# Kernel tuning notes

Measured on AMD Instinct MI355X. Metric: run time of the kernel, lower is better.

## Reference

```python
import jax, jax.numpy as jnp
import numpy as np
import math

N, CIN, COUT, K, H, W = 16, 512, 512, 1024, 64, 64


def setup_inputs() -> dict:
    key = jax.random.key(0)
    k0, k1, k2, k3, k4 = jax.random.split(key, 5)
    latent = jax.random.normal(k0, (N, CIN, H, W), dtype=jnp.float32)
    # kaiming_uniform_ on (K, COUT): bound = sqrt(6 / fan_in), fan_in = COUT
    cb_bound = math.sqrt(6.0 / COUT)
    codebook = jax.random.uniform(k1, (K, COUT), minval=-cb_bound, maxval=cb_bound, dtype=jnp.float32)
    # nn.Linear default init: uniform(-1/sqrt(fan_in), 1/sqrt(fan_in)), weight stored (out, in)
    wq = jax.random.uniform(k2, (COUT, CIN), minval=-1 / math.sqrt(CIN), maxval=1 / math.sqrt(CIN), dtype=jnp.float32)
    wk = jax.random.uniform(k3, (COUT, COUT), minval=-1 / math.sqrt(COUT), maxval=1 / math.sqrt(COUT), dtype=jnp.float32)
    wv = jax.random.uniform(k4, (COUT, COUT), minval=-1 / math.sqrt(COUT), maxval=1 / math.sqrt(COUT), dtype=jnp.float32)
    return {"latent": latent, "codebook": codebook, "wq": wq, "wk": wk, "wv": wv, "temperature": 1}


def _forward(latent, codebook, wq, wk, wv, temperature):
    n, cin, h, w = latent.shape
    kk, cout = codebook.shape
    scale = math.sqrt(cin)

    q = jnp.einsum("nchw,oc->nhwo", latent, wq)          # [n,h,w,cout]
    kmat = codebook @ wk.T                                   # [k,cout]
    v = codebook @ wv.T                                      # [k,cout]
    logit = jnp.einsum("nhwc,kc->nhwk", q, kmat) / scale  # [n,h,w,k]

    # ---- no-grad mask / histogram computation (dropout branch) ----
    lg = jax.lax.stop_gradient(logit)
    rk = jax.random.key(1234)
    r1, r2, r3 = jax.random.split(rk, 3)
    prob = jax.nn.softmax(lg, axis=-1)
    prob = jnp.where(prob < 1.0 / kk, 0.0, prob)
    mask = jax.random.bernoulli(r1, prob)                    # [n,h,w,k] bool
    trueCode = jnp.argmax(prob, axis=-1)                     # [n,h,w] int
    flat = trueCode.reshape(n, -1)
    binCount = jnp.zeros((n, kk), dtype=jnp.float32).at[jnp.arange(n)[:, None], flat].add(1.0)
    frequency = binCount[jnp.arange(n)[:, None, None], trueCode]  # [n,h,w]
    dropout = jax.random.bernoulli(r2, frequency / float(h * w))   # [n,h,w] bool
    scatterMask = jax.nn.one_hot(trueCode, kk, dtype=jnp.bool_) & dropout[..., None]
    mask = mask | scatterMask

    maskedLogit = jnp.where(mask, -1e9, logit)

    # ---- hard gumbel-softmax (straight-through) ----
    g = jax.random.gumbel(r3, maskedLogit.shape, dtype=maskedLogit.dtype)
    y_soft = jax.nn.softmax((maskedLogit + g) / temperature, axis=-1)
    y_hard = jax.nn.one_hot(jnp.argmax(y_soft, axis=-1), kk, dtype=y_soft.dtype)
    sample = y_hard - jax.lax.stop_gradient(y_soft) + y_soft

    result = jnp.einsum("nhwk,kc->nhwc", sample, v)
    quantized = jnp.transpose(result, (0, 3, 1, 2))          # [n,cout,h,w]
    code = jnp.argmax(sample, axis=-1)
    return quantized, code, logit, trueCode, frequency, binCount


def reference(latent, codebook, wq, wk, wv, temperature):
    return _forward(latent, codebook, wq, wk, wv, temperature)
```

## Files before the change

kernel.cpp:

```cpp
#include <hip/hip_runtime.h>
#include <stdint.h>
#include <stddef.h>

#define NB   16
#define CIN  512
#define COUT 512
#define KK   1024

#define MARGIN    2e-5f
#define INV_SCALE 0.04419417382415922f

typedef short short4v __attribute__((ext_vector_type(4)));
typedef short short8v __attribute__((ext_vector_type(8)));
typedef float f32x4  __attribute__((ext_vector_type(4)));

union Frag { short4v h[2]; short8v v8; };

__host__ __device__ inline void tf2x32(uint32_t k0, uint32_t k1,
                                       uint32_t x0, uint32_t x1,
                                       uint32_t& o0, uint32_t& o1) {
  uint32_t ks2 = k0 ^ k1 ^ 0x1BD11BDAu;
  x0 += k0; x1 += k1;
#define TF_RND(r) { x0 += x1; x1 = (x1 << r) | (x1 >> (32 - r)); x1 ^= x0; }
  TF_RND(13) TF_RND(15) TF_RND(26) TF_RND(6)
  x0 += k1;  x1 += ks2 + 1u;
  TF_RND(17) TF_RND(29) TF_RND(16) TF_RND(24)
  x0 += ks2; x1 += k0 + 2u;
  TF_RND(13) TF_RND(15) TF_RND(26) TF_RND(6)
  x0 += k0;  x1 += k1 + 3u;
  TF_RND(17) TF_RND(29) TF_RND(16) TF_RND(24)
  x0 += k1;  x1 += ks2 + 4u;
  TF_RND(13) TF_RND(15) TF_RND(26) TF_RND(6)
  x0 += ks2; x1 += k0 + 5u;
#undef TF_RND
  o0 = x0; o1 = x1;
}

__device__ inline float bits_to_u(uint32_t b) {
  return __uint_as_float((b >> 9) | 0x3f800000u) - 1.0f;
}

__device__ __host__ inline uint16_t f2bf(float f) {
  union { float f; uint32_t u; } c; c.f = f;
  uint32_t r = (c.u + 0x7fffu + ((c.u >> 16) & 1u)) >> 16;
  return (uint16_t)r;
}
__device__ inline float bf2f(uint16_t h) {
  union { uint32_t u; float f; } c; c.u = ((uint32_t)h) << 16;
  return c.f;
}

__device__ inline int permpos(int c) {
  const int base32 = c & ~31, within = c & 31;
  const int g = (within >> 2) & 3;
  const int e = (within & 16) ? (4 + (within & 3)) : (within & 3);
  return base32 + g * 8 + e;
}

__global__ __launch_bounds__(256) void k_prep(const float* __restrict__ cb,
                                              const float* __restrict__ wk,
                                              const float* __restrict__ wv,
                                              double* __restrict__ kmatT64,
                                              float* __restrict__ v) {
  __shared__ __align__(16) float rows[4][CIN];
  const int k0 = blockIdx.x * 4;
  const int t = threadIdx.x;
#pragma unroll
  for (int kk = 0; kk < 4; ++kk)
    for (int c = t; c < CIN; c += 256) rows[kk][c] = cb[(size_t)(k0 + kk) * CIN + c];
  __syncthreads();
#pragma unroll
  for (int oo = 0; oo < 2; ++oo) {
    const int o = t + oo * 256;
    const float* kr = wk + (size_t)o * CIN;
    const float* vr = wv + (size_t)o * CIN;
    double ak[4] = {0, 0, 0, 0}, av[4] = {0, 0, 0, 0};
    for (int c = 0; c < CIN; c += 4) {
      const float4 k4 = *(const float4*)(kr + c);
      const float4 v4 = *(const float4*)(vr + c);
#pragma unroll
      for (int kk = 0; kk < 4; ++kk) {
        const float4 c4 = *(const float4*)&rows[kk][c];
        ak[kk] += (double)c4.x * (double)k4.x + (double)c4.y * (double)k4.y
                + (double)c4.z * (double)k4.z + (double)c4.w * (double)k4.w;
        av[kk] += (double)c4.x * (double)v4.x + (double)c4.y * (double)v4.y
                + (double)c4.z * (double)v4.z + (double)c4.w * (double)v4.w;
      }
    }
#pragma unroll
    for (int kk = 0; kk < 4; ++kk) {
      kmatT64[(size_t)o * KK + k0 + kk] = ak[kk];
      v[(size_t)(k0 + kk) * COUT + o]  = (float)av[kk];
    }
  }
}

__global__ __launch_bounds__(256) void k_wfold(const float* __restrict__ wq,
                                               const double* __restrict__ kmatT64,
                                               double* __restrict__ WT64,
                                               uint16_t* __restrict__ Wph,
                                               uint16_t* __restrict__ Wpl) {
  __shared__ __align__(16) float  As[16][64];
  __shared__ __align__(16) double Bs[16][128];
  const int t  = threadIdx.x;
  const int cb = (blockIdx.x >> 3) * 64;
  const int kb = (blockIdx.x & 7) * 128;
  const int tc = t >> 4, tk = t & 15;

  double acc[4][8];
#pragma unroll
  for (int i = 0; i < 4; ++i)
#pragma unroll
    for (int j = 0; j < 8; ++j) acc[i][j] = 0.0;

  for (int o0 = 0; o0 < COUT; o0 += 16) {
    {
      const int o2 = t >> 4, c4 = (t & 15) * 4;
      float4 f = *(const float4*)&wq[(size_t)(o0 + o2) * CIN + cb + c4];
      As[o2][c4+0] = f.x; As[o2][c4+1] = f.y; As[o2][c4+2] = f.z; As[o2][c4+3] = f.w;
    }
    {
      const int o2 = t >> 4, k8 = (t & 15) * 8;
      const double* src = &kmatT64[(size_t)(o0 + o2) * KK + kb + k8];
#pragma unroll
      for (int j = 0; j < 8; ++j) Bs[o2][k8 + j] = src[j];
    }
    __syncthreads();
#pragma unroll 4
    for (int o2 = 0; o2 < 16; ++o2) {
      double a[4], b[8];
#pragma unroll
      for (int i = 0; i < 4; ++i) a[i] = (double)As[o2][tc*4 + i];
#pragma unroll
      for (int j = 0; j < 8; ++j) b[j] = Bs[o2][tk*8 + j];
#pragma unroll
      for (int i = 0; i < 4; ++i)
#pragma unroll
        for (int j = 0; j < 8; ++j) acc[i][j] += a[i] * b[j];
    }
    __syncthreads();
  }
#pragma unroll
  for (int i = 0; i < 4; ++i) {
    const int c = cb + tc*4 + i;
    const int pp = permpos(c);
#pragma unroll
    for (int j = 0; j < 8; ++j) {
      const int k = kb + tk*8 + j;
      const double a = acc[i][j];
      WT64[(size_t)k * CIN + c] = a;
      const float wf = (float)a;
      const uint16_t hb = f2bf(wf);
      const float lof = wf - bf2f(hb);
      Wph[(size_t)k * CIN + pp] = hb;
      Wpl[(size_t)k * CIN + pp] = f2bf(lof);
    }
  }
}

__global__ __launch_bounds__(256) void k_aprep(const float* __restrict__ latent,
                                               uint16_t* __restrict__ Apk) {
  __shared__ float T[128][68];
  const int rb = blockIdx.x, n = rb >> 6, h = rb & 63, t = threadIdx.x;
  for (int c0 = 0; c0 < 512; c0 += 128) {
    const int c2 = t >> 1, wh = (t & 1) * 32;
    const float* src = latent + (size_t)n * 2097152 + (size_t)(c0 + c2) * 4096 + h * 64 + wh;
#pragma unroll
    for (int i = 0; i < 8; ++i)
      *(float4*)&T[c2][wh + i*4] = *(const float4*)(src + i*4);
    __syncthreads();
    const int w = t & 63, cp = t >> 6;
    const int cs = (c0 >> 5) + cp;
    const int p = rb * 64 + w;
    uint16_t* dst = Apk + ((size_t)cs * 65536 + p) * 64;
#pragma unroll
    for (int q = 0; q < 8; ++q) {
      short8v vv;
#pragma unroll
      for (int j = 0; j < 4; ++j) {
        const float f = T[cp*32 + (q & 3) * 4 + (q >> 2) * 16 + j][w];
        const uint16_t hb = f2bf(f);
        vv[j]     = (short)hb;
        vv[4 + j] = (short)f2bf(f - bf2f(hb));
      }
      *(short8v*)(dst + q * 8) = vv;
    }
    __syncthreads();
  }
}

#define STAGE_B(buf_, st_) do {                                            \
  const int kc_ = (st_) >> 4, cs_ = (st_) & 15;                            \
  _Pragma("unroll")                                                        \
  for (int i_ = 0; i_ < 8; ++i_) {                                         \
    const int half_ = i_ >> 2;                                             \
    const int Dl_ = (i_ & 3) * 4096 + wave * 1024 + lane * 16;             \
    const int kcol_ = Dl_ >> 6;                                            \
    const int bs_ = ((Dl_ >> 4) & 3) ^ ((kcol_ >> 1) & 3);                 \
    const uint16_t* gsrc_ = (half_ ? Wpl : Wph) +                          \
        ((size_t)(kc_ * 256 + kcol_) * 512 + cs_ * 32 + bs_ * 8);          \
    uint16_t* ldst_ = &Bst[buf_][half_ * 8192 + (Dl_ >> 1)];               \
    __builtin_amdgcn_global_load_lds(                                      \
        (const __attribute__((address_space(1))) uint32_t*)gsrc_,          \
        (__attribute__((address_space(3))) uint32_t*)ldst_, 16, 0, 0);     \
  } } while (0)

#define STAGE_A(buf_, st_) do {                                            \
  const int cs_ = (st_) & 15;                                              \
  _Pragma("unroll")                                                        \
  for (int i_ = 0; i_ < 2; ++i_) {                                         \
    const int D_ = i_ * 4096 + t * 16;                                     \
    const int row_ = D_ >> 7;                                              \
    const int q_ = ((D_ >> 4) & 7) ^ (row_ & 7);                           \
    const uint16_t* gsrc_ = Apk +                                          \
        ((size_t)cs_ * 65536 + pbase + row_) * 64 + q_ * 8;                \
    uint16_t* ldst_ = &Ast[buf_][D_ >> 1];                                 \
    __builtin_amdgcn_global_load_lds(                                      \
        (const __attribute__((address_space(1))) uint32_t*)gsrc_,          \
        (__attribute__((address_space(3))) uint32_t*)ldst_, 16, 0, 0);     \
  } } while (0)

__global__ __launch_bounds__(256, 2) void k_logit(
    const uint16_t* __restrict__ Apk,
    const uint16_t* __restrict__ Wph, const uint16_t* __restrict__ Wpl,
    const float* __restrict__ latent, const double* __restrict__ WT64,
    float* __restrict__ out_logit, int* __restrict__ trueCode, int* __restrict__ binCnt) {
  __shared__ __align__(16) char smem[81920];
  uint16_t (*Bst)[16384] = (uint16_t(*)[16384])smem;
  uint16_t (*Ast)[4096]  = (uint16_t(*)[4096])(smem + 65536);
  float* rowBv   = (float*)(smem + 65536);
  int*   rowBk   = (int*)  (smem + 65536 + 256);
  int*   candCnt = (int*)  (smem + 65536 + 512);
  int  (*candK)[8] = (int(*)[8])(smem + 65536 + 768);

  const int t = threadIdx.x;
  const int wave = t >> 6, lane = t & 63;
  const int wr = wave >> 1, wc = wave & 1;
  const int rb = blockIdx.x, n = rb >> 6, h = rb & 63;
  const int pbase = rb * 64;
  const int lg = lane >> 4, l15 = lane & 15;

  float bestv[2][4]; int bestk[2][4];
#pragma unroll
  for (int rt = 0; rt < 2; ++rt)
#pragma unroll
    for (int reg = 0; reg < 4; ++reg) { bestv[rt][reg] = -1.0e30f; bestk[rt][reg] = 0; }

  f32x4 acc[2][8];

  STAGE_A(0, 0);
  STAGE_B(0, 0);
  __syncthreads();

  for (int st = 0; st < 64; ++st) {
    const int cur = st & 1, kc = st >> 4, cs = st & 15;
    if (cs == 0) {
#pragma unroll
      for (int rt = 0; rt < 2; ++rt)
#pragma unroll
        for (int ct = 0; ct < 8; ++ct) acc[rt][ct] = (f32x4){0.f, 0.f, 0.f, 0.f};
    }
    if (st < 63) { STAGE_A(cur ^ 1, st + 1); STAGE_B(cur ^ 1, st + 1); }

    Frag ah[2], al[2];
#pragma unroll
    for (int rt = 0; rt < 2; ++rt) {
      const int row = wr * 32 + rt * 16 + l15;
      const uint16_t* ab = &Ast[cur][row * 64];
      const int s0 = (lg ^ (row & 7)) * 8;
      Frag f0, f1;
      f0.v8 = *(const short8v*)(ab + s0);
      f1.v8 = *(const short8v*)(ab + (s0 ^ 32));
      ah[rt].h[0] = f0.h[0]; ah[rt].h[1] = f1.h[0];
      al[rt].h[0] = f0.h[1]; al[rt].h[1] = f1.h[1];
    }

#pragma unroll
    for (int ct = 0; ct < 8; ++ct) {
      const int kcol = wc * 128 + ct * 16 + l15;
      const int sw = lg ^ ((kcol >> 1) & 3);
      Frag bh, bl;
      bh.v8 = *(const short8v*)&Bst[cur][kcol * 32 + sw * 8];
      bl.v8 = *(const short8v*)&Bst[cur][8192 + kcol * 32 + sw * 8];
#pragma unroll
      for (int rt = 0; rt < 2; ++rt) {
        acc[rt][ct] = __builtin_amdgcn_mfma_f32_16x16x32_bf16(ah[rt].v8, bh.v8, acc[rt][ct], 0, 0, 0);
        acc[rt][ct] = __builtin_amdgcn_mfma_f32_16x16x32_bf16(ah[rt].v8, bl.v8, acc[rt][ct], 0, 0, 0);
        acc[rt][ct] = __builtin_amdgcn_mfma_f32_16x16x32_bf16(al[rt].v8, bh.v8, acc[rt][ct], 0, 0, 0);
      }
    }
    if (cs == 15) {
#pragma unroll
      for (int rt = 0; rt < 2; ++rt) {
#pragma unroll
        for (int reg = 0; reg < 4; ++reg) {
          const int prow = pbase + wr * 32 + rt * 16 + 4 * lg + reg;
          float* dst = out_logit + (size_t)prow * KK + kc * 256 + wc * 128 + l15;
#pragma unroll
          for (int ct = 0; ct < 8; ++ct) {
            const float v = acc[rt][ct][reg] * INV_SCALE;
            dst[ct * 16] = v;
            if (v > bestv[rt][reg]) { bestv[rt][reg] = v; bestk[rt][reg] = kc * 256 + wc * 128 + ct * 16 + l15; }
          }
        }
      }
    }
    __syncthreads();
  }

#pragma unroll
  for (int rt = 0; rt < 2; ++rt)
#pragma unroll
    for (int reg = 0; reg < 4; ++reg) {
      float v = bestv[rt][reg]; int k = bestk[rt][reg];
#pragma unroll
      for (int off = 1; off < 16; off <<= 1) {
        const float ov = __shfl_xor(v, off);
        const int   ok = __shfl_xor(k, off);
        if (ov > v || (ov == v && ok < k)) { v = ov; k = ok; }
      }
      bestv[rt][reg] = v; bestk[rt][reg] = k;
    }
  if (l15 == 0 && wc == 0) {
#pragma unroll
    for (int rt = 0; rt < 2; ++rt)
#pragma unroll
      for (int reg = 0; reg < 4; ++reg) {
        const int r = wr * 32 + rt * 16 + 4 * lg + reg;
        rowBv[r] = bestv[rt][reg]; rowBk[r] = bestk[rt][reg];
      }
  }
  if (t < 64) candCnt[t] = 0;
  __syncthreads();
  if (l15 == 0 && wc == 1) {
#pragma unroll
    for (int rt = 0; rt < 2; ++rt)
#pragma unroll
      for (int reg = 0; reg < 4; ++reg) {
        const int r = wr * 32 + rt * 16 + 4 * lg + reg;
        const float v = bestv[rt][reg]; const int k = bestk[rt][reg];
        if (v > rowBv[r] || (v == rowBv[r] && k < rowBk[r])) { rowBv[r] = v; rowBk[r] = k; }
      }
  }
  __syncthreads();

  {
    const int r = t >> 2, qd = t & 3;
    const size_t base = (size_t)(pbase + r) * KK + qd * 256;
    const float thr = rowBv[r] - MARGIN;
    for (int x = 0; x < 64; ++x) {
      const float4 f = *(const float4*)&out_logit[base + x * 4];
      const int kb = qd * 256 + x * 4;
      if (f.x >= thr) { int id = atomicAdd(&candCnt[r], 1); if (id < 8) candK[r][id] = kb + 0; }
      if (f.y >= thr) { int id = atomicAdd(&candCnt[r], 1); if (id < 8) candK[r][id] = kb + 1; }
      if (f.z >= thr) { int id = atomicAdd(&candCnt[r], 1); if (id < 8) candK[r][id] = kb + 2; }
      if (f.w >= thr) { int id = atomicAdd(&candCnt[r], 1); if (id < 8) candK[r][id] = kb + 3; }
    }
  }
  __syncthreads();

  const float* Ab = latent + (size_t)n * CIN * 4096 + h * 64;
  const int wv = t >> 6, lane_ = t & 63;
  for (int rr = 0; rr < 16; ++rr) {
    const int r = wv * 16 + rr;
    const int p = pbase + r;
    int cnt = candCnt[r]; if (cnt > 8) cnt = 8;
    if (cnt <= 1) {
      if (lane_ == 0) {
        const int tc0 = rowBk[r];
        trueCode[p] = tc0;
        atomicAdd(&binCnt[n * KK + tc0], 1);
      }
    } else {
      int ks[8];
#pragma unroll
      for (int m = 0; m < 8; ++m) ks[m] = candK[r][m < cnt ? m : 0];
      double part[8] = {0, 0, 0, 0, 0, 0, 0, 0};
#pragma unroll
      for (int jj = 0; jj < 8; ++jj) {
        const int c = jj * 64 + lane_;
        const double lv = (double)Ab[(size_t)c * 4096 + r];
#pragma unroll
        for (int m = 0; m < 8; ++m)
          if (m < cnt) part[m] += lv * WT64[(size_t)ks[m] * CIN + c];
      }
#pragma unroll
      for (int m = 0; m < 8; ++m)
        for (int off = 32; off; off >>= 1) part[m] += __shfl_xor(part[m], off);
      if (lane_ == 0) {
        double bv = -1.0e300; int bkk = KK;
#pragma unroll
        for (int m = 0; m < 8; ++m)
          if (m < cnt && (part[m] > bv || (part[m] == bv && ks[m] < bkk))) { bv = part[m]; bkk = ks[m]; }
        trueCode[p] = bkk;
        atomicAdd(&binCnt[n * KK + bkk], 1);
      }
    }
  }
}

__global__ __launch_bounds__(256) void k_final(const float* __restrict__ logit,
                                               const int* __restrict__ trueCode,
                                               const int* __restrict__ binCnt,
                                               float* __restrict__ out_code,
                                               float* __restrict__ out_tc,
                                               float* __restrict__ out_freq,
                                               int* __restrict__ code_int,
                                               uint32_t r1a, uint32_t r1b,
                                               uint32_t r2a, uint32_t r2b,
                                               uint32_t r3a, uint32_t r3b) {
  const int lane = threadIdx.x & 63;
  const int p = blockIdx.x * 4 + (threadIdx.x >> 6);
  const float* Lr = logit + (size_t)p * KK + lane * 16;

  float l[16];
#pragma unroll
  for (int i = 0; i < 4; ++i) {
    const float4 f = *(const float4*)(Lr + i * 4);
    l[i*4+0] = f.x; l[i*4+1] = f.y; l[i*4+2] = f.z; l[i*4+3] = f.w;
  }

  float m = l[0];
#pragma unroll
  for (int i = 1; i < 16; ++i) m = fmaxf(m, l[i]);
  for (int off = 32; off; off >>= 1) m = fmaxf(m, __shfl_xor(m, off));

  float e[16], s = 0.f;
#pragma unroll
  for (int i = 0; i < 16; ++i) { e[i] = __expf(l[i] - m); s += e[i]; }
  for (int off = 32; off; off >>= 1) s += __shfl_xor(s, off);

  const int tc = trueCode[p];
  const float fq = (float)binCnt[(p >> 12) * KK + tc];
  uint32_t d0, d1; tf2x32(r2a, r2b, 0u, (uint32_t)p, d0, d1);
  const bool drop = bits_to_u(d0 ^ d1) < fq * (1.0f / 4096.0f);

  const float thr = s * 0.0009765625f;
  float bv = -3.0e38f; int bk = 0;
#pragma unroll
  for (int j = 0; j < 16; ++j) {
    const int k = lane * 16 + j;
    const uint32_t idx = (uint32_t)(p * KK + k);
    uint32_t m0, m1, g0, g1;
    tf2x32(r1a, r1b, 0u, idx, m0, m1);
    tf2x32(r3a, r3b, 0u, idx, g0, g1);
    const bool mk = ((e[j] >= thr) && (bits_to_u(m0 ^ m1) * s < e[j])) || (k == tc && drop);
    const float u3  = fmaxf(bits_to_u(g0 ^ g1), 1.17549435082228751e-38f);
    const float gum = -__logf(-logf(u3));
    const float z = mk ? (gum - 1.0e9f) : (l[j] + gum);
    if (z > bv) { bv = z; bk = k; }
  }
  for (int off = 32; off; off >>= 1) {
    const float ov = __shfl_xor(bv, off);
    const int   ok = __shfl_xor(bk, off);
    if (ov > bv || (ov == bv && ok < bk)) { bv = ov; bk = ok; }
  }
  if (lane == 0) {
    out_code[p] = (float)bk; code_int[p] = bk;
    out_tc[p] = (float)tc;   out_freq[p] = fq;
  }
}

__global__ __launch_bounds__(256) void k_quant(const float* __restrict__ v,
                                               const int* __restrict__ code_int,
                                               float* __restrict__ outq) {
  const int rb = blockIdx.x;
  const int n = rb >> 6, h = rb & 63;
  const int t = threadIdx.x;
  __shared__ int codes[64];
  if (t < 64) codes[t] = code_int[rb * 64 + t];
  __syncthreads();
  const int w = t & 63, og = t >> 6;
  const float* vr = v + (size_t)codes[w] * COUT;
  float* ob = outq + (size_t)n * COUT * 4096 + (size_t)h * 64 + w;
  for (int o = og * 128; o < og * 128 + 128; ++o)
    ob[(size_t)o * 4096] = vr[o];
}

__global__ __launch_bounds__(256) void k_bincopy(const int* __restrict__ binCnt,
                                                 float* __restrict__ outb) {
  const int i = blockIdx.x * 256 + threadIdx.x;
  if (i < NB * KK) outb[i] = (float)binCnt[i];
}

extern "C" void kernel_launch(void* const* d_in, const int* in_sizes, int n_in,
                              void* d_out, int out_size, void* d_ws, size_t ws_size,
                              hipStream_t stream) {
  const float* latent   = (const float*)d_in[0];
  const float* codebook = (const float*)d_in[1];
  const float* wq       = (const float*)d_in[2];
  const float* wk       = (const float*)d_in[3];
  const float* wv       = (const float*)d_in[4];

  float* out = (float*)d_out;
  float* out_quant = out;
  float* out_code  = out + 33554432;
  float* out_logit = out + 33619968;
  float* out_tc    = out + 100728832;
  float* out_freq  = out + 100794368;
  float* out_bin   = out + 100859904;

  double*   WT64 = (double*)  out_quant;
  uint16_t* Wph  = (uint16_t*)(out_quant + 1048576);
  uint16_t* Wpl  = (uint16_t*)(out_quant + 1310720);

  char* ws = (char*)d_ws;
  uint16_t* Apk     = (uint16_t*)(ws);
  double*   kmatT64 = (double*)(ws);
  float*    v       = (float*)(ws + 134217728);
  int*      trueCode= (int*)  (ws + 136314880);
  int*      code_int= (int*)  (ws + 136577024);
  int*      binCnt  = (int*)  (ws + 136839168);

  uint32_t r1a, r1b, r2a, r2b, r3a, r3b;
  tf2x32(0u, 1234u, 0u, 0u, r1a, r1b);
  tf2x32(0u, 1234u, 0u, 1u, r2a, r2b);
  tf2x32(0u, 1234u, 0u, 2u, r3a, r3b);

  hipMemsetAsync(binCnt, 0, NB * KK * sizeof(int), stream);
  k_prep  <<<256,   256, 0, stream>>>(codebook, wk, wv, kmatT64, v);
  k_wfold <<<64,    256, 0, stream>>>(wq, kmatT64, WT64, Wph, Wpl);
  k_aprep <<<1024,  256, 0, stream>>>(latent, Apk);
  k_logit <<<1024,  256, 0, stream>>>(Apk, Wph, Wpl, latent, WT64,
                                      out_logit, trueCode, binCnt);
  k_final <<<16384, 256, 0, stream>>>(out_logit, trueCode, binCnt,
                                      out_code, out_tc, out_freq, code_int,
                                      r1a, r1b, r2a, r2b, r3a, r3b);
  k_quant <<<1024,  256, 0, stream>>>(v, code_int, out_quant);
  k_bincopy<<<64,   256, 0, stream>>>(binCnt, out_bin);
}
```

Before: 988.9 us.

## Fuse codebook prep with latent packing, track top-2 logits, coalesce quant writes

Merges the codebook projection kernel and the latent bf16 packing kernel into one launch, with kmatT64 moved into the output buffer so it no longer aliases Apk in the workspace. The logit kernel now tracks the top-2 logits per row and only rescans the logit row when the gap is under the margin, which skips the full candidate scan for most rows. The quantize kernel is restructured so each block writes contiguous float4 runs along the spatial axis. The cost is more registers for the top-2 bookkeeping and a gather pattern on v in the quant kernel.

```diff
diff --git a/kernel.cpp b/kernel.cpp
--- a/kernel.cpp
+++ b/kernel.cpp
@@ -57,40 +57,73 @@
   return base32 + g * 8 + e;
 }
 
-__global__ __launch_bounds__(256) void k_prep(const float* __restrict__ cb,
-                                              const float* __restrict__ wk,
-                                              const float* __restrict__ wv,
-                                              double* __restrict__ kmatT64,
-                                              float* __restrict__ v) {
-  __shared__ __align__(16) float rows[4][CIN];
-  const int k0 = blockIdx.x * 4;
+__global__ __launch_bounds__(256) void k_combo(const float* __restrict__ cb,
+                                               const float* __restrict__ wk,
+                                               const float* __restrict__ wv,
+                                               const float* __restrict__ latent,
+                                               double* __restrict__ kmatT64,
+                                               float* __restrict__ v,
+                                               uint16_t* __restrict__ Apk) {
+  __shared__ __align__(16) char sm[34816];
   const int t = threadIdx.x;
-#pragma unroll
-  for (int kk = 0; kk < 4; ++kk)
-    for (int c = t; c < CIN; c += 256) rows[kk][c] = cb[(size_t)(k0 + kk) * CIN + c];
-  __syncthreads();
-#pragma unroll
-  for (int oo = 0; oo < 2; ++oo) {
-    const int o = t + oo * 256;
-    const float* kr = wk + (size_t)o * CIN;
-    const float* vr = wv + (size_t)o * CIN;
-    double ak[4] = {0, 0, 0, 0}, av[4] = {0, 0, 0, 0};
-    for (int c = 0; c < CIN; c += 4) {
-      const float4 k4 = *(const float4*)(kr + c);
-      const float4 v4 = *(const float4*)(vr + c);
-#pragma unroll
-      for (int kk = 0; kk < 4; ++kk) {
-        const float4 c4 = *(const float4*)&rows[kk][c];
-        ak[kk] += (double)c4.x * (double)k4.x + (double)c4.y * (double)k4.y
-                + (double)c4.z * (double)k4.z + (double)c4.w * (double)k4.w;
-        av[kk] += (double)c4.x * (double)v4.x + (double)c4.y * (double)v4.y
-                + (double)c4.z * (double)v4.z + (double)c4.w * (double)v4.w;
-      }
-    }
-#pragma unroll
-    for (int kk = 0; kk < 4; ++kk) {
-      kmatT64[(size_t)o * KK + k0 + kk] = ak[kk];
-      v[(size_t)(k0 + kk) * COUT + o]  = (float)av[kk];
+  if (blockIdx.x < 128) {
+    float (*rows)[CIN] = (float(*)[CIN])sm;
+    const int k0 = blockIdx.x * 8;
+#pragma unroll
+    for (int kk = 0; kk < 8; ++kk)
+      for (int c = t; c < CIN; c += 256) rows[kk][c] = cb[(size_t)(k0 + kk) * CIN + c];
+    __syncthreads();
+#pragma unroll
+    for (int oo = 0; oo < 2; ++oo) {
+      const int o = t + oo * 256;
+      const float* kr = wk + (size_t)o * CIN;
+      const float* vr = wv + (size_t)o * CIN;
+      double ak[8] = {0,0,0,0,0,0,0,0}, av[8] = {0,0,0,0,0,0,0,0};
+      for (int c = 0; c < CIN; c += 4) {
+        const float4 k4 = *(const float4*)(kr + c);
+        const float4 v4 = *(const float4*)(vr + c);
+#pragma unroll
+        for (int kk = 0; kk < 8; ++kk) {
+          const float4 c4 = *(const float4*)&rows[kk][c];
+          ak[kk] += (double)c4.x * (double)k4.x + (double)c4.y * (double)k4.y
+                  + (double)c4.z * (double)k4.z + (double)c4.w * (double)k4.w;
+          av[kk] += (double)c4.x * (double)v4.x + (double)c4.y * (double)v4.y
+                  + (double)c4.z * (double)v4.z + (double)c4.w * (double)v4.w;
+        }
+      }
+#pragma unroll
+      for (int kk = 0; kk < 8; ++kk) {
+        kmatT64[(size_t)o * KK + k0 + kk] = ak[kk];
+        v[(size_t)(k0 + kk) * COUT + o]  = (float)av[kk];
+      }
+    }
+  } else {
+    float (*T)[68] = (float(*)[68])sm;
+    const int rb = blockIdx.x - 128, n = rb >> 6, h = rb & 63;
+    for (int c0 = 0; c0 < 512; c0 += 128) {
+      const int c2 = t >> 1, wh = (t & 1) * 32;
+      const float* src = latent + (size_t)n * 2097152 + (size_t)(c0 + c2) * 4096 + h * 64 + wh;
+#pragma unroll
+      for (int i = 0; i < 8; ++i)
+        *(float4*)&T[c2][wh + i*4] = *(const float4*)(src + i*4);
+      __syncthreads();
+      const int w = t & 63, cp = t >> 6;
+      const int cs = (c0 >> 5) + cp;
+      const int p = rb * 64 + w;
+      uint16_t* dst = Apk + ((size_t)cs * 65536 + p) * 64;
+#pragma unroll
+      for (int q = 0; q < 8; ++q) {
+        short8v vv;
+#pragma unroll
+        for (int j = 0; j < 4; ++j) {
+          const float f = T[cp*32 + (q & 3) * 4 + (q >> 2) * 16 + j][w];
+          const uint16_t hb = f2bf(f);
+          vv[j]     = (short)hb;
+          vv[4 + j] = (short)f2bf(f - bf2f(hb));
+        }
+        *(short8v*)(dst + q * 8) = vv;
+      }
+      __syncthreads();
     }
   }
 }
@@ -158,48 +191,17 @@
   }
 }
 
-__global__ __launch_bounds__(256) void k_aprep(const float* __restrict__ latent,
-                                               uint16_t* __restrict__ Apk) {
-  __shared__ float T[128][68];
-  const int rb = blockIdx.x, n = rb >> 6, h = rb & 63, t = threadIdx.x;
-  for (int c0 = 0; c0 < 512; c0 += 128) {
-    const int c2 = t >> 1, wh = (t & 1) * 32;
-    const float* src = latent + (size_t)n * 2097152 + (size_t)(c0 + c2) * 4096 + h * 64 + wh;
-#pragma unroll
-    for (int i = 0; i < 8; ++i)
-      *(float4*)&T[c2][wh + i*4] = *(const float4*)(src + i*4);
-    __syncthreads();
-    const int w = t & 63, cp = t >> 6;
-    const int cs = (c0 >> 5) + cp;
-    const int p = rb * 64 + w;
-    uint16_t* dst = Apk + ((size_t)cs * 65536 + p) * 64;
-#pragma unroll
-    for (int q = 0; q < 8; ++q) {
-      short8v vv;
-#pragma unroll
-      for (int j = 0; j < 4; ++j) {
-        const float f = T[cp*32 + (q & 3) * 4 + (q >> 2) * 16 + j][w];
-        const uint16_t hb = f2bf(f);
-        vv[j]     = (short)hb;
-        vv[4 + j] = (short)f2bf(f - bf2f(hb));
-      }
-      *(short8v*)(dst + q * 8) = vv;
-    }
-    __syncthreads();
-  }
-}
-
 #define STAGE_B(buf_, st_) do {                                            \
   const int kc_ = (st_) >> 4, cs_ = (st_) & 15;                            \
   _Pragma("unroll")                                                        \
   for (int i_ = 0; i_ < 8; ++i_) {                                         \
     const int half_ = i_ >> 2;                                             \
-    const int Dl_ = (i_ & 3) * 4096 + wave * 1024 + lane * 16;             \
-    const int kcol_ = Dl_ >> 6;                                            \
-    const int bs_ = ((Dl_ >> 4) & 3) ^ ((kcol_ >> 1) & 3);                 \
+    const int D_ = (i_ & 3) * 4096 + wave * 1024 + lane * 16;              \
+    const int kcol_ = D_ >> 6;                                             \
+    const int bs_ = ((D_ >> 4) & 3) ^ ((kcol_ >> 1) & 3);                  \
     const uint16_t* gsrc_ = (half_ ? Wpl : Wph) +                          \
         ((size_t)(kc_ * 256 + kcol_) * 512 + cs_ * 32 + bs_ * 8);          \
-    uint16_t* ldst_ = &Bst[buf_][half_ * 8192 + (Dl_ >> 1)];               \
+    uint16_t* ldst_ = &Bst[buf_][half_ * 8192 + (D_ >> 1)];                \
     __builtin_amdgcn_global_load_lds(                                      \
         (const __attribute__((address_space(1))) uint32_t*)gsrc_,          \
         (__attribute__((address_space(3))) uint32_t*)ldst_, 16, 0, 0);     \
@@ -228,23 +230,28 @@
   __shared__ __align__(16) char smem[81920];
   uint16_t (*Bst)[16384] = (uint16_t(*)[16384])smem;
   uint16_t (*Ast)[4096]  = (uint16_t(*)[4096])(smem + 65536);
-  float* rowBv   = (float*)(smem + 65536);
-  int*   rowBk   = (int*)  (smem + 65536 + 256);
-  int*   candCnt = (int*)  (smem + 65536 + 512);
-  int  (*candK)[8] = (int(*)[8])(smem + 65536 + 768);
+  float* rv1     = (float*)(smem + 65536);
+  int*   rk1     = (int*)  (smem + 65536 + 256);
+  float* rv2     = (float*)(smem + 65536 + 512);
+  int*   rk2     = (int*)  (smem + 65536 + 768);
+  int*   candCnt = (int*)  (smem + 65536 + 1024);
+  int  (*candK)[8] = (int(*)[8])(smem + 65536 + 1280);
 
   const int t = threadIdx.x;
   const int wave = t >> 6, lane = t & 63;
   const int wr = wave >> 1, wc = wave & 1;
-  const int rb = blockIdx.x, n = rb >> 6, h = rb & 63;
+  const int rb = blockIdx.x, n = rb >> 6;
   const int pbase = rb * 64;
   const int lg = lane >> 4, l15 = lane & 15;
 
-  float bestv[2][4]; int bestk[2][4];
+  float v1_[2][4], v2_[2][4]; int k1_[2][4], k2_[2][4];
 #pragma unroll
   for (int rt = 0; rt < 2; ++rt)
 #pragma unroll
-    for (int reg = 0; reg < 4; ++reg) { bestv[rt][reg] = -1.0e30f; bestk[rt][reg] = 0; }
+    for (int reg = 0; reg < 4; ++reg) {
+      v1_[rt][reg] = -3.0e38f; k1_[rt][reg] = 0x7fffffff;
+      v2_[rt][reg] = -3.0e38f; k2_[rt][reg] = 0x7fffffff;
+    }
 
   f32x4 acc[2][8];
 
@@ -296,12 +303,18 @@
         for (int reg = 0; reg < 4; ++reg) {
           const int prow = pbase + wr * 32 + rt * 16 + 4 * lg + reg;
           float* dst = out_logit + (size_t)prow * KK + kc * 256 + wc * 128 + l15;
+          float v1 = v1_[rt][reg], v2 = v2_[rt][reg];
+          int   k1 = k1_[rt][reg], k2 = k2_[rt][reg];
 #pragma unroll
           for (int ct = 0; ct < 8; ++ct) {
-            const float v = acc[rt][ct][reg] * INV_SCALE;
-            dst[ct * 16] = v;
-            if (v > bestv[rt][reg]) { bestv[rt][reg] = v; bestk[rt][reg] = kc * 256 + wc * 128 + ct * 16 + l15; }
+            const float vv = acc[rt][ct][reg] * INV_SCALE;
+            dst[ct * 16] = vv;
+            const int kk = kc * 256 + wc * 128 + ct * 16 + l15;
+            if (vv > v1 || (vv == v1 && kk < k1)) { v2 = v1; k2 = k1; v1 = vv; k1 = kk; }
+            else if (vv > v2 || (vv == v2 && kk < k2)) { v2 = vv; k2 = kk; }
           }
+          v1_[rt][reg] = v1; v2_[rt][reg] = v2;
+          k1_[rt][reg] = k1; k2_[rt][reg] = k2;
         }
       }
     }
@@ -312,66 +325,99 @@
   for (int rt = 0; rt < 2; ++rt)
 #pragma unroll
     for (int reg = 0; reg < 4; ++reg) {
-      float v = bestv[rt][reg]; int k = bestk[rt][reg];
+      float v1 = v1_[rt][reg], v2 = v2_[rt][reg];
+      int   k1 = k1_[rt][reg], k2 = k2_[rt][reg];
 #pragma unroll
       for (int off = 1; off < 16; off <<= 1) {
-        const float ov = __shfl_xor(v, off);
-        const int   ok = __shfl_xor(k, off);
-        if (ov > v || (ov == v && ok < k)) { v = ov; k = ok; }
-      }
-      bestv[rt][reg] = v; bestk[rt][reg] = k;
-    }
-  if (l15 == 0 && wc == 0) {
+        const float o1 = __shfl_xor(v1, off); const int ok1 = __shfl_xor(k1, off);
+        const float o2 = __shfl_xor(v2, off); const int ok2 = __shfl_xor(k2, off);
+        const bool aw = (v1 > o1) || (v1 == o1 && k1 < ok1);
+        float n1, n2; int nk1, nk2;
+        if (aw) {
+          n1 = v1; nk1 = k1;
+          if ((o1 > v2) || (o1 == v2 && ok1 < k2)) { n2 = o1; nk2 = ok1; }
+          else { n2 = v2; nk2 = k2; }
+        } else {
+          n1 = o1; nk1 = ok1;
+          if ((v1 > o2) || (v1 == o2 && k1 < ok2)) { n2 = v1; nk2 = k1; }
+          else { n2 = o2; nk2 = ok2; }
+        }
+        v1 = n1; k1 = nk1; v2 = n2; k2 = nk2;
+      }
+      v1_[rt][reg] = v1; v2_[rt][reg] = v2;
+      k1_[rt][reg] = k1; k2_[rt][reg] = k2;
+    }
+  if (wc == 0 && l15 == 0) {
 #pragma unroll
     for (int rt = 0; rt < 2; ++rt)
 #pragma unroll
       for (int reg = 0; reg < 4; ++reg) {
         const int r = wr * 32 + rt * 16 + 4 * lg + reg;
-        rowBv[r] = bestv[rt][reg]; rowBk[r] = bestk[rt][reg];
-      }
-  }
-  if (t < 64) candCnt[t] = 0;
+        rv1[r] = v1_[rt][reg]; rk1[r] = k1_[rt][reg];
+        rv2[r] = v2_[rt][reg]; rk2[r] = k2_[rt][reg];
+      }
+  }
   __syncthreads();
-  if (l15 == 0 && wc == 1) {
+  if (wc == 1 && l15 == 0) {
 #pragma unroll
     for (int rt = 0; rt < 2; ++rt)
 #pragma unroll
       for (int reg = 0; reg < 4; ++reg) {
         const int r = wr * 32 + rt * 16 + 4 * lg + reg;
-        const float v = bestv[rt][reg]; const int k = bestk[rt][reg];
-        if (v > rowBv[r] || (v == rowBv[r] && k < rowBk[r])) { rowBv[r] = v; rowBk[r] = k; }
+        const float a1 = rv1[r], a2 = rv2[r];
+        const int   ak1 = rk1[r], ak2 = rk2[r];
+        const float b1 = v1_[rt][reg], b2 = v2_[rt][reg];
+        const int   bk1 = k1_[rt][reg], bk2 = k2_[rt][reg];
+        const bool aw = (a1 > b1) || (a1 == b1 && ak1 < bk1);
+        float n1, n2; int nk1, nk2;
+        if (aw) {
+          n1 = a1; nk1 = ak1;
+          if ((b1 > a2) || (b1 == a2 && bk1 < ak2)) { n2 = b1; nk2 = bk1; }
+          else { n2 = a2; nk2 = ak2; }
+        } else {
+          n1 = b1; nk1 = bk1;
+          if ((a1 > b2) || (a1 == b2 && ak1 < bk2)) { n2 = a1; nk2 = ak1; }
+          else { n2 = b2; nk2 = bk2; }
+        }
+        rv1[r] = n1; rk1[r] = nk1; rv2[r] = n2; rk2[r] = nk2;
       }
   }
   __syncthreads();
 
-  {
-    const int r = t >> 2, qd = t & 3;
-    const size_t base = (size_t)(pbase + r) * KK + qd * 256;
-    const float thr = rowBv[r] - MARGIN;
-    for (int x = 0; x < 64; ++x) {
-      const float4 f = *(const float4*)&out_logit[base + x * 4];
-      const int kb = qd * 256 + x * 4;
-      if (f.x >= thr) { int id = atomicAdd(&candCnt[r], 1); if (id < 8) candK[r][id] = kb + 0; }
-      if (f.y >= thr) { int id = atomicAdd(&candCnt[r], 1); if (id < 8) candK[r][id] = kb + 1; }
-      if (f.z >= thr) { int id = atomicAdd(&candCnt[r], 1); if (id < 8) candK[r][id] = kb + 2; }
-      if (f.w >= thr) { int id = atomicAdd(&candCnt[r], 1); if (id < 8) candK[r][id] = kb + 3; }
-    }
-  }
-  __syncthreads();
-
-  const float* Ab = latent + (size_t)n * CIN * 4096 + h * 64;
   const int wv = t >> 6, lane_ = t & 63;
   for (int rr = 0; rr < 16; ++rr) {
     const int r = wv * 16 + rr;
     const int p = pbase + r;
-    int cnt = candCnt[r]; if (cnt > 8) cnt = 8;
-    if (cnt <= 1) {
+    const float mv1 = rv1[r], mv2 = rv2[r];
+    if (mv1 - mv2 > MARGIN) {
       if (lane_ == 0) {
-        const int tc0 = rowBk[r];
+        const int tc0 = rk1[r];
         trueCode[p] = tc0;
         atomicAdd(&binCnt[n * KK + tc0], 1);
       }
     } else {
+      if (lane_ == 0) candCnt[r] = 0;
+      __builtin_amdgcn_sched_barrier(0);
+      asm volatile("s_waitcnt lgkmcnt(0)" ::: "memory");
+      __builtin_amdgcn_sched_barrier(0);
+      {
+        const float thr = mv1 - MARGIN;
+        const float* src = out_logit + (size_t)p * KK + lane_ * 16;
+#pragma unroll
+        for (int i = 0; i < 4; ++i) {
+          const float4 f = *(const float4*)(src + i * 4);
+          const int kb = lane_ * 16 + i * 4;
+          if (f.x >= thr) { int id = atomicAdd(&candCnt[r], 1); if (id < 8) candK[r][id] = kb + 0; }
+          if (f.y >= thr) { int id = atomicAdd(&candCnt[r], 1); if (id < 8) candK[r][id] = kb + 1; }
+          if (f.z >= thr) { int id = atomicAdd(&candCnt[r], 1); if (id < 8) candK[r][id] = kb + 2; }
+          if (f.w >= thr) { int id = atomicAdd(&candCnt[r], 1); if (id < 8) candK[r][id] = kb + 3; }
+        }
+      }
+      __builtin_amdgcn_sched_barrier(0);
+      asm volatile("s_waitcnt lgkmcnt(0)" ::: "memory");
+      __builtin_amdgcn_sched_barrier(0);
+      int cnt = candCnt[r]; if (cnt > 8) cnt = 8;
+      const float* Ap = latent + (size_t)(p >> 12) * 2097152 + (p & 4095);
       int ks[8];
 #pragma unroll
       for (int m = 0; m < 8; ++m) ks[m] = candK[r][m < cnt ? m : 0];
@@ -379,7 +425,7 @@
 #pragma unroll
       for (int jj = 0; jj < 8; ++jj) {
         const int c = jj * 64 + lane_;
-        const double lv = (double)Ab[(size_t)c * 4096 + r];
+        const double lv = (double)Ap[(size_t)c * 4096];
 #pragma unroll
         for (int m = 0; m < 8; ++m)
           if (m < cnt) part[m] += lv * WT64[(size_t)ks[m] * CIN + c];
@@ -464,17 +510,29 @@
 __global__ __launch_bounds__(256) void k_quant(const float* __restrict__ v,
                                                const int* __restrict__ code_int,
                                                float* __restrict__ outq) {
-  const int rb = blockIdx.x;
-  const int n = rb >> 6, h = rb & 63;
+  __shared__ int codes[4096];
+  const int n  = blockIdx.x >> 6;
+  const int og = blockIdx.x & 63;
   const int t = threadIdx.x;
-  __shared__ int codes[64];
-  if (t < 64) codes[t] = code_int[rb * 64 + t];
+  const int4* cp = (const int4*)(code_int + (size_t)n * 4096);
+#pragma unroll
+  for (int i = 0; i < 4; ++i) ((int4*)codes)[t + i * 256] = cp[t + i * 256];
   __syncthreads();
-  const int w = t & 63, og = t >> 6;
-  const float* vr = v + (size_t)codes[w] * COUT;
-  float* ob = outq + (size_t)n * COUT * 4096 + (size_t)h * 64 + w;
-  for (int o = og * 128; o < og * 128 + 128; ++o)
-    ob[(size_t)o * 4096] = vr[o];
+  float* ob = outq + ((size_t)n * 512 + og * 8) * 4096;
+  for (int c = 0; c < 4; ++c) {
+    const int pos4 = (c * 256 + t) * 4;
+    const int c0 = codes[pos4], c1 = codes[pos4 + 1], c2 = codes[pos4 + 2], c3 = codes[pos4 + 3];
+    const float* v0 = v + (size_t)c0 * COUT;
+    const float* v1 = v + (size_t)c1 * COUT;
+    const float* v2 = v + (size_t)c2 * COUT;
+    const float* v3 = v + (size_t)c3 * COUT;
+#pragma unroll
+    for (int oo = 0; oo < 8; ++oo) {
+      const int o = og * 8 + oo;
+      float4 val = make_float4(v0[o], v1[o], v2[o], v3[o]);
+      *(float4*)(ob + (size_t)oo * 4096 + pos4) = val;
+    }
+  }
 }
 
 __global__ __launch_bounds__(256) void k_bincopy(const int* __restrict__ binCnt,
@@ -500,13 +558,13 @@
   float* out_freq  = out + 100794368;
   float* out_bin   = out + 100859904;
 
-  double*   WT64 = (double*)  out_quant;
-  uint16_t* Wph  = (uint16_t*)(out_quant + 1048576);
-  uint16_t* Wpl  = (uint16_t*)(out_quant + 1310720);
+  double*   WT64    = (double*)  out_quant;
+  uint16_t* Wph     = (uint16_t*)(out_quant + 1048576);
+  uint16_t* Wpl     = (uint16_t*)(out_quant + 1310720);
+  double*   kmatT64 = (double*)  (out_quant + 1572864);
 
   char* ws = (char*)d_ws;
   uint16_t* Apk     = (uint16_t*)(ws);
-  double*   kmatT64 = (double*)(ws);
   float*    v       = (float*)(ws + 134217728);
   int*      trueCode= (int*)  (ws + 136314880);
   int*      code_int= (int*)  (ws + 136577024);
@@ -518,9 +576,8 @@
   tf2x32(0u, 1234u, 0u, 2u, r3a, r3b);
 
   hipMemsetAsync(binCnt, 0, NB * KK * sizeof(int), stream);
-  k_prep  <<<256,   256, 0, stream>>>(codebook, wk, wv, kmatT64, v);
+  k_combo <<<1152,  256, 0, stream>>>(codebook, wk, wv, latent, kmatT64, v, Apk);
   k_wfold <<<64,    256, 0, stream>>>(wq, kmatT64, WT64, Wph, Wpl);
-  k_aprep <<<1024,  256, 0, stream>>>(latent, Apk);
   k_logit <<<1024,  256, 0, stream>>>(Apk, Wph, Wpl, latent, WT64,
                                       out_logit, trueCode, binCnt);
   k_final <<<16384, 256, 0, stream>>>(out_logit, trueCode, binCnt,
```

Measured after the change: 909.2 us. -8.1%, faster.
